# Performance work log

Hardware: AMD Instinct MI355X
Metric: run time of the kernel (lower is better)

Reference implementation:

```python
import jax, jax.numpy as jnp
import numpy as np

H = 16       # num_heads
DH = 64      # dim_head
SCALE = DH ** -0.5


def setup_inputs() -> dict:
    key = jax.random.key(0)
    k1, k2 = jax.random.split(key)
    ZT = jax.random.normal(k1, (2, 2048, 1024), dtype=jnp.float32)
    # Linear weight, shape (H*dh, dim); scaled like a typical init for stability
    W = jax.random.normal(k2, (1024, 1024), dtype=jnp.float32) * 0.02
    return {"ZT": ZT, "W": W}


def reference(ZT, W):
    b, n, dim = ZT.shape
    # UT(ZT): ZT @ W^T -> (b, n, H*dh), reshape to (b, h, n, dh)
    ZTU = jnp.einsum('bnd,ed->bne', ZT, W).reshape(b, n, H, DH).transpose(0, 2, 1, 3)
    # scores = ZTU @ ZTU^T * scale  (b, h, n, n)
    scores = jnp.einsum('bhnd,bhmd->bhnm', ZTU, ZTU) * SCALE
    attn = jax.nn.softmax(scores, axis=-1)  # dropout p=0 -> identity
    # attn @ ZTU -> (b, h, n, dh) -> (b, n, H*dh)
    ssa = jnp.einsum('bhnm,bhmd->bhnd', attn, ZTU)
    ssa = ssa.transpose(0, 2, 1, 3).reshape(b, n, H * DH)
    # UT(I).T == W (shape (H*dh, dim)); final projection back to dim
    mssa = jnp.einsum('bne,ed->bnd', ssa, W)
    # return_proj=False path: module returns (MSSA_out, MSSA_out)
    return (mssa, mssa)
```

## Files before the change

kernel.cpp:

```cpp
#include <hip/hip_runtime.h>
#include <hip/hip_bf16.h>
#include <stdint.h>

typedef __attribute__((ext_vector_type(8))) short bf16x8;
typedef __attribute__((ext_vector_type(4))) float f32x4;

#define MFMA16(a, b, c) __builtin_amdgcn_mfma_f32_16x16x32_bf16(a, b, c, 0, 0, 0)

typedef const __attribute__((address_space(1))) unsigned int* as1_u32p;
typedef __attribute__((address_space(3))) unsigned int* as3_u32p;
__device__ __forceinline__ void gl_lds16(const void* g, void* l) {
    __builtin_amdgcn_global_load_lds((as1_u32p)g, (as3_u32p)l, 16, 0, 0);
}

__device__ __forceinline__ unsigned short f2bs(float f) {
    __hip_bfloat16 h = __float2bfloat16(f);
    unsigned short s;
    __builtin_memcpy(&s, &h, 2);
    return s;
}

__device__ __forceinline__ unsigned int pk_bf16(float a, float b) {
    float2 f; f.x = a; f.y = b;
    __hip_bfloat162 h = __float22bfloat162_rn(f);
    unsigned int u;
    __builtin_memcpy(&u, &h, 4);
    return u;
}

__device__ __forceinline__ float exp2_raw(float x) {
    float r;
    asm("v_exp_f32 %0, %1" : "=v"(r) : "v"(x));
    return r;
}

#define QSCALE 0.18033688f

__global__ __launch_bounds__(256) void cvt_w_k(const float* __restrict__ w,
                                               unsigned short* __restrict__ wbf,
                                               unsigned short* __restrict__ wtbf) {
    __shared__ __attribute__((aligned(16))) unsigned short T[64 * 72];
    const int b2 = blockIdx.x;
    const int tid = threadIdx.x;
    const int e0 = (b2 >> 4) * 64, d0 = (b2 & 15) * 64;
    const int el = tid >> 2;
    const int dl = (tid & 3) * 16;
    const float* src = w + (size_t)(e0 + el) * 1024 + d0 + dl;
    unsigned short myv[16];
#pragma unroll
    for (int q = 0; q < 4; ++q) {
        const float4 v = *(const float4*)(src + q * 4);
        myv[q * 4 + 0] = f2bs(v.x);
        myv[q * 4 + 1] = f2bs(v.y);
        myv[q * 4 + 2] = f2bs(v.z);
        myv[q * 4 + 3] = f2bs(v.w);
    }
    *(bf16x8*)(wbf + (size_t)(e0 + el) * 1024 + d0 + dl) = *(const bf16x8*)&myv[0];
    *(bf16x8*)(wbf + (size_t)(e0 + el) * 1024 + d0 + dl + 8) = *(const bf16x8*)&myv[8];
#pragma unroll
    for (int q = 0; q < 16; ++q) T[(dl + q) * 72 + el] = myv[q];
    __syncthreads();
#pragma unroll
    for (int p = 0; p < 2; ++p) {
        const int idx = p * 256 + tid;
        const int dd = idx >> 3, c = (idx & 7) * 8;
        const bf16x8 v = *(const bf16x8*)&T[dd * 72 + c];
        *(bf16x8*)(wtbf + (size_t)(d0 + dd) * 1024 + e0 + c) = v;
    }
}

template <int EPI>
__global__ __launch_bounds__(256, 2) void gemm_bt_k(
    const float* __restrict__ Af32, const __hip_bfloat16* __restrict__ Abf,
    const __hip_bfloat16* __restrict__ B,
    unsigned short* __restrict__ ztu, unsigned short* __restrict__ ztut,
    float* __restrict__ out0, float* __restrict__ out1) {
    __shared__ __attribute__((aligned(16))) unsigned short smem[12288];
    unsigned short* At = smem;
    unsigned short* Bt = smem + 4096;
    unsigned short* Tb = smem;

    const int p = blockIdx.x;
    const int bm = (p & 7) * 8 + ((p >> 3) & 7);
    const int bn = p >> 6;
    const int tid = threadIdx.x;
    const int wave = tid >> 6, lane = tid & 63;
    const int wm = wave >> 1, wn = wave & 1;
    const int quad = lane >> 4, l16 = lane & 15;

    f32x4 acc[2][4] = {};

    const int lr = lane >> 2, lc = (lane & 3) * 8;
    const float* Agf = Af32 ? Af32 + (size_t)(bm * 64 + wave * 16 + lr) * 1024 + lc : nullptr;
    const __hip_bfloat16* Agb =
        Abf ? Abf + (size_t)(bm * 64 + wave * 16 + lr) * 1024 + lc : nullptr;
    const __hip_bfloat16* Bg0 = B + (size_t)(bn * 128 + (2 * wave) * 16 + lr) * 1024 + lc;
    const __hip_bfloat16* Bg1 = B + (size_t)(bn * 128 + (2 * wave + 1) * 16 + lr) * 1024 + lc;
    unsigned short* lA = At + wave * 512;
    unsigned short* lB0 = Bt + (2 * wave) * 512;
    unsigned short* lB1 = Bt + (2 * wave + 1) * 512;

    for (int kt = 0; kt < 16; ++kt) {
        const int ko = kt << 6;
        if (EPI == 0) {
#pragma unroll
            for (int h = 0; h < 2; ++h) {
                const float4 v0 = *(const float4*)(Agf + ko + h * 32);
                const float4 v1 = *(const float4*)(Agf + ko + h * 32 + 4);
                uint4 wv;
                wv.x = pk_bf16(v0.x, v0.y);
                wv.y = pk_bf16(v0.z, v0.w);
                wv.z = pk_bf16(v1.x, v1.y);
                wv.w = pk_bf16(v1.z, v1.w);
                *(uint4*)(lA + h * 2048 + lr * 32 + lc) = wv;
            }
        } else {
            gl_lds16(Agb + ko, lA);
            gl_lds16(Agb + ko + 32, lA + 2048);
        }
        gl_lds16(Bg0 + ko, lB0);
        gl_lds16(Bg0 + ko + 32, lB0 + 4096);
        gl_lds16(Bg1 + ko, lB1);
        gl_lds16(Bg1 + ko + 32, lB1 + 4096);
        __syncthreads();
        bf16x8 af[2][2], bfr[2][4];
#pragma unroll
        for (int h = 0; h < 2; ++h)
#pragma unroll
            for (int i = 0; i < 2; ++i)
                af[h][i] = *(const bf16x8*)&At[h * 2048 + (wm * 32 + i * 16 + l16) * 32 + quad * 8];
#pragma unroll
        for (int h = 0; h < 2; ++h)
#pragma unroll
            for (int j = 0; j < 4; ++j)
                bfr[h][j] = *(const bf16x8*)&Bt[h * 4096 + (wn * 64 + j * 16 + l16) * 32 + quad * 8];
#pragma unroll
        for (int h = 0; h < 2; ++h)
#pragma unroll
            for (int i = 0; i < 2; ++i)
#pragma unroll
                for (int j = 0; j < 4; ++j) acc[i][j] = MFMA16(af[h][i], bfr[h][j], acc[i][j]);
        __syncthreads();
    }

    if (EPI == 0) {
        const int h = bn * 2 + wn;
        const int bb = bm >> 5;
        const int nb = (bm & 31) * 64;
        const size_t hb = (size_t)(bb * 16 + h) * 131072;
#pragma unroll
        for (int i = 0; i < 2; ++i) {
#pragma unroll
            for (int r = 0; r < 4; ++r) {
                const int n = nb + wm * 32 + i * 16 + quad * 4 + r;
                uint2 pk;
                pk.x = pk_bf16(acc[i][0][r], acc[i][1][r]);
                pk.y = pk_bf16(acc[i][2][r], acc[i][3][r]);
                *(uint2*)(ztu + hb + n * 64 + l16 * 4) = pk;
                const int npl = wm * 32 + quad * 8 + i * 4 + r;
                Tb[(wn * 64 + 0 + l16) * 72 + npl] = (unsigned short)(pk.x & 0xffff);
                Tb[(wn * 64 + 16 + l16) * 72 + npl] = (unsigned short)(pk.x >> 16);
                Tb[(wn * 64 + 32 + l16) * 72 + npl] = (unsigned short)(pk.y & 0xffff);
                Tb[(wn * 64 + 48 + l16) * 72 + npl] = (unsigned short)(pk.y >> 16);
            }
        }
        __syncthreads();
#pragma unroll
        for (int ee = 0; ee < 4; ++ee) {
            const int e_local = wave * 32 + ee * 8 + (lane >> 3);
            const int nc = (lane & 7) * 8;
            const bf16x8 v = *(const bf16x8*)&Tb[e_local * 72 + nc];
            const int hh = bn * 2 + (e_local >> 6);
            const int dh = e_local & 63;
            *(bf16x8*)(ztut + (size_t)(bb * 16 + hh) * 131072 + dh * 2048 + nb + nc) = v;
        }
    } else {
#pragma unroll
        for (int i = 0; i < 2; ++i) {
#pragma unroll
            for (int r = 0; r < 4; ++r) {
                const int mm = bm * 64 + wm * 32 + i * 16 + quad * 4 + r;
#pragma unroll
                for (int j = 0; j < 4; ++j) {
                    const int e = bn * 128 + wn * 64 + j * 16 + l16;
                    const float v = acc[i][j][r];
                    out0[(size_t)mm * 1024 + e] = v;
                    out1[(size_t)mm * 1024 + e] = v;
                }
            }
        }
    }
}

__global__ __launch_bounds__(256, 2) void attn_k(const unsigned short* __restrict__ ztu,
                                                 const unsigned short* __restrict__ ztut,
                                                 unsigned short* __restrict__ ssa) {
    __shared__ __attribute__((aligned(16))) unsigned short Kt[64 * 64];
    __shared__ __attribute__((aligned(16))) unsigned short Vt[64 * 64];
    const int p = blockIdx.x;
    const int ii = p >> 3;
    const int bh = (p & 7) * 4 + (ii >> 4);
    const int qt = ii & 15;
    const int tid = threadIdx.x, wave = tid >> 6, lane = tid & 63;
    const int quad = lane >> 4, l16 = lane & 15;
    const unsigned short* base = ztu + (size_t)bh * 131072;
    const unsigned short* baseT = ztut + (size_t)bh * 131072;

    const int qb = qt * 128 + wave * 32;
    bf16x8 qa[2][2];
#pragma unroll
    for (int g = 0; g < 2; ++g) {
        qa[g][0] = *(const bf16x8*)(base + (qb + g * 16 + l16) * 64 + quad * 8);
        qa[g][1] = *(const bf16x8*)(base + (qb + g * 16 + l16) * 64 + 32 + quad * 8);
    }

    float lsum[2] = {0.f, 0.f};
    f32x4 o[2][4] = {};

    const int c0 = wave * 2, c1 = c0 + 1;
    const int lrow = lane >> 3;
    const int sw = (lane & 7) ^ lrow;
    const unsigned short* gK0 = base + (c0 * 8 + lrow) * 64 + sw * 8;
    const unsigned short* gK1 = base + (c1 * 8 + lrow) * 64 + sw * 8;
    const unsigned short* gV0 = baseT + (size_t)(c0 * 8 + lrow) * 2048 + sw * 8;
    const unsigned short* gV1 = baseT + (size_t)(c1 * 8 + lrow) * 2048 + sw * 8;
    unsigned short* lK0 = &Kt[c0 * 512];
    unsigned short* lK1 = &Kt[c1 * 512];
    unsigned short* lV0 = &Vt[c0 * 512];
    unsigned short* lV1 = &Vt[c1 * 512];

    const int swq = (quad ^ (l16 & 7));
    const int koff0 = l16 * 64 + swq * 8;
    const int koff1 = l16 * 64 + (swq ^ 4) * 8;

    for (int t = 0; t < 32; ++t) {
        gl_lds16(gK0 + t * 4096, lK0);
        gl_lds16(gK1 + t * 4096, lK1);
        gl_lds16(gV0 + t * 64, lV0);
        gl_lds16(gV1 + t * 64, lV1);
        __syncthreads();

        f32x4 st[2][4];
#pragma unroll
        for (int nf = 0; nf < 4; ++nf) {
            bf16x8 kb0 = *(const bf16x8*)&Kt[nf * 1024 + koff0];
            bf16x8 kb1 = *(const bf16x8*)&Kt[nf * 1024 + koff1];
#pragma unroll
            for (int g = 0; g < 2; ++g) {
                f32x4 z = {0.f, 0.f, 0.f, 0.f};
                z = MFMA16(kb0, qa[g][0], z);
                z = MFMA16(kb1, qa[g][1], z);
                st[g][nf] = z;
            }
        }

        bf16x8 pa[2][2];
#pragma unroll
        for (int g = 0; g < 2; ++g) {
            float e[16];
#pragma unroll
            for (int nf = 0; nf < 4; ++nf)
#pragma unroll
                for (int r = 0; r < 4; ++r) e[nf * 4 + r] = exp2_raw(st[g][nf][r] * QSCALE);
            float s0 = 0.f, s1 = 0.f;
#pragma unroll
            for (int q = 0; q < 8; ++q) { s0 += e[q]; s1 += e[q + 8]; }
            lsum[g] += s0 + s1;
            uint4 u0, u1;
            u0.x = pk_bf16(e[0], e[1]);   u0.y = pk_bf16(e[2], e[3]);
            u0.z = pk_bf16(e[4], e[5]);   u0.w = pk_bf16(e[6], e[7]);
            u1.x = pk_bf16(e[8], e[9]);   u1.y = pk_bf16(e[10], e[11]);
            u1.z = pk_bf16(e[12], e[13]); u1.w = pk_bf16(e[14], e[15]);
            __builtin_memcpy(&pa[g][0], &u0, 16);
            __builtin_memcpy(&pa[g][1], &u1, 16);
        }

#pragma unroll
        for (int df = 0; df < 4; ++df) {
            bf16x8 vb0 = *(const bf16x8*)&Vt[df * 1024 + koff0];
            bf16x8 vb1 = *(const bf16x8*)&Vt[df * 1024 + koff1];
#pragma unroll
            for (int g = 0; g < 2; ++g) {
                o[g][df] = MFMA16(vb0, pa[g][0], o[g][df]);
                o[g][df] = MFMA16(vb1, pa[g][1], o[g][df]);
            }
        }
        __syncthreads();
    }

    const int b = bh >> 4, h = bh & 15;
#pragma unroll
    for (int g = 0; g < 2; ++g) {
        float v = lsum[g];
        v += __shfl_xor(v, 16);
        v += __shfl_xor(v, 32);
        const float inv = 1.0f / v;
        const int token = b * 2048 + qb + g * 16 + l16;
#pragma unroll
        for (int df = 0; df < 4; ++df) {
            uint2 pk;
            pk.x = pk_bf16(o[g][df][0] * inv, o[g][df][1] * inv);
            pk.y = pk_bf16(o[g][df][2] * inv, o[g][df][3] * inv);
            *(uint2*)(ssa + (size_t)token * 1024 + h * 64 + df * 16 + quad * 4) = pk;
        }
    }
}

extern "C" void kernel_launch(void* const* d_in, const int* in_sizes, int n_in,
                              void* d_out, int out_size, void* d_ws, size_t ws_size,
                              hipStream_t stream) {
    const float* ZT = (const float*)d_in[0];
    const float* W = (const float*)d_in[1];
    float* out = (float*)d_out;
    char* ws = (char*)d_ws;

    unsigned short* wbf   = (unsigned short*)(ws);
    unsigned short* wtbf  = (unsigned short*)(ws + 2u * 1024 * 1024);
    unsigned short* ztu   = (unsigned short*)(ws + 4u * 1024 * 1024);
    unsigned short* ztut  = (unsigned short*)(ws + 12u * 1024 * 1024);
    unsigned short* ssabf = (unsigned short*)(ws + 20u * 1024 * 1024);

    cvt_w_k<<<256, 256, 0, stream>>>(W, wbf, wtbf);
    gemm_bt_k<0><<<512, 256, 0, stream>>>(ZT, nullptr, (const __hip_bfloat16*)wbf, ztu, ztut,
                                          nullptr, nullptr);
    attn_k<<<512, 256, 0, stream>>>(ztu, ztut, ssabf);
    gemm_bt_k<1><<<512, 256, 0, stream>>>(nullptr, (const __hip_bfloat16*)ssabf,
                                          (const __hip_bfloat16*)wtbf, nullptr, nullptr, out,
                                          out + 4194304);
}
```

Measured before the change: 158.7 us.

## Pre-convert ZT to bf16 and double-buffer swizzled LDS staging in GEMMs

ZT is now converted to bf16 in a widened conversion kernel, so the first GEMM can load A with direct global-to-LDS copies like the second GEMM. The GEMM main loop double-buffers LDS and prefetches the next K tile while computing the current one, using a 64-wide K tile with an XOR-swizzled layout to avoid bank conflicts. The cost is an extra fp32 read and bf16 write of ZT in a separate pass, plus twice the LDS per block, which may reduce occupancy.

```diff
diff --git a/kernel.cpp b/kernel.cpp
--- a/kernel.cpp
+++ b/kernel.cpp
@@ -36,12 +36,26 @@
 
 #define QSCALE 0.18033688f
 
-__global__ __launch_bounds__(256) void cvt_w_k(const float* __restrict__ w,
-                                               unsigned short* __restrict__ wbf,
-                                               unsigned short* __restrict__ wtbf) {
+__global__ __launch_bounds__(256) void cvt_k(const float* __restrict__ w,
+                                             const float* __restrict__ zt,
+                                             unsigned short* __restrict__ wbf,
+                                             unsigned short* __restrict__ wtbf,
+                                             unsigned short* __restrict__ ztbf) {
     __shared__ __attribute__((aligned(16))) unsigned short T[64 * 72];
+    const int tid = threadIdx.x;
+    if (blockIdx.x >= 256) {
+        const int i = ((int)blockIdx.x - 256) * 2048 + tid * 8;
+        const float4 v0 = *(const float4*)(zt + i);
+        const float4 v1 = *(const float4*)(zt + i + 4);
+        uint4 wv;
+        wv.x = pk_bf16(v0.x, v0.y);
+        wv.y = pk_bf16(v0.z, v0.w);
+        wv.z = pk_bf16(v1.x, v1.y);
+        wv.w = pk_bf16(v1.z, v1.w);
+        *(uint4*)(ztbf + i) = wv;
+        return;
+    }
     const int b2 = blockIdx.x;
-    const int tid = threadIdx.x;
     const int e0 = (b2 >> 4) * 64, d0 = (b2 & 15) * 64;
     const int el = tid >> 2;
     const int dl = (tid & 3) * 16;
@@ -71,13 +85,10 @@
 
 template <int EPI>
 __global__ __launch_bounds__(256, 2) void gemm_bt_k(
-    const float* __restrict__ Af32, const __hip_bfloat16* __restrict__ Abf,
-    const __hip_bfloat16* __restrict__ B,
+    const __hip_bfloat16* __restrict__ Abf, const __hip_bfloat16* __restrict__ B,
     unsigned short* __restrict__ ztu, unsigned short* __restrict__ ztut,
     float* __restrict__ out0, float* __restrict__ out1) {
-    __shared__ __attribute__((aligned(16))) unsigned short smem[12288];
-    unsigned short* At = smem;
-    unsigned short* Bt = smem + 4096;
+    __shared__ __attribute__((aligned(16))) unsigned short smem[24576];
     unsigned short* Tb = smem;
 
     const int p = blockIdx.x;
@@ -90,50 +101,46 @@
 
     f32x4 acc[2][4] = {};
 
-    const int lr = lane >> 2, lc = (lane & 3) * 8;
-    const float* Agf = Af32 ? Af32 + (size_t)(bm * 64 + wave * 16 + lr) * 1024 + lc : nullptr;
-    const __hip_bfloat16* Agb =
-        Abf ? Abf + (size_t)(bm * 64 + wave * 16 + lr) * 1024 + lc : nullptr;
-    const __hip_bfloat16* Bg0 = B + (size_t)(bn * 128 + (2 * wave) * 16 + lr) * 1024 + lc;
-    const __hip_bfloat16* Bg1 = B + (size_t)(bn * 128 + (2 * wave + 1) * 16 + lr) * 1024 + lc;
-    unsigned short* lA = At + wave * 512;
-    unsigned short* lB0 = Bt + (2 * wave) * 512;
-    unsigned short* lB1 = Bt + (2 * wave + 1) * 512;
+    const int lrow = lane >> 3;
+    const int sw = (lane & 7) ^ lrow;
+    const __hip_bfloat16* Ag0 = Abf + (size_t)(bm * 64 + (2 * wave) * 8 + lrow) * 1024 + sw * 8;
+    const __hip_bfloat16* Ag1 = Ag0 + 8 * 1024;
+    const __hip_bfloat16* Bg0 = B + (size_t)(bn * 128 + (4 * wave) * 8 + lrow) * 1024 + sw * 8;
+    const __hip_bfloat16* Bg1 = Bg0 + 8 * 1024;
+    const __hip_bfloat16* Bg2 = Bg0 + 16 * 1024;
+    const __hip_bfloat16* Bg3 = Bg0 + 24 * 1024;
+
+    auto stage = [&](int ko, unsigned short* sb) {
+        gl_lds16(Ag0 + ko, sb + (2 * wave) * 512);
+        gl_lds16(Ag1 + ko, sb + (2 * wave + 1) * 512);
+        gl_lds16(Bg0 + ko, sb + 4096 + (4 * wave) * 512);
+        gl_lds16(Bg1 + ko, sb + 4096 + (4 * wave + 1) * 512);
+        gl_lds16(Bg2 + ko, sb + 4096 + (4 * wave + 2) * 512);
+        gl_lds16(Bg3 + ko, sb + 4096 + (4 * wave + 3) * 512);
+    };
+
+    const int ch0 = (quad ^ (l16 & 7)) * 8;
+    const int ch1 = ch0 ^ 32;
+    const int raA = (wm * 32 + l16) * 64;
+    const int raB = (wn * 64 + l16) * 64;
+
+    stage(0, smem);
+    __syncthreads();
 
     for (int kt = 0; kt < 16; ++kt) {
-        const int ko = kt << 6;
-        if (EPI == 0) {
-#pragma unroll
-            for (int h = 0; h < 2; ++h) {
-                const float4 v0 = *(const float4*)(Agf + ko + h * 32);
-                const float4 v1 = *(const float4*)(Agf + ko + h * 32 + 4);
-                uint4 wv;
-                wv.x = pk_bf16(v0.x, v0.y);
-                wv.y = pk_bf16(v0.z, v0.w);
-                wv.z = pk_bf16(v1.x, v1.y);
-                wv.w = pk_bf16(v1.z, v1.w);
-                *(uint4*)(lA + h * 2048 + lr * 32 + lc) = wv;
-            }
-        } else {
-            gl_lds16(Agb + ko, lA);
-            gl_lds16(Agb + ko + 32, lA + 2048);
-        }
-        gl_lds16(Bg0 + ko, lB0);
-        gl_lds16(Bg0 + ko + 32, lB0 + 4096);
-        gl_lds16(Bg1 + ko, lB1);
-        gl_lds16(Bg1 + ko + 32, lB1 + 4096);
-        __syncthreads();
+        unsigned short* const sb = smem + (kt & 1) * 12288;
+        if (kt < 15) stage((kt + 1) << 6, smem + (((kt & 1) ^ 1) * 12288));
         bf16x8 af[2][2], bfr[2][4];
 #pragma unroll
-        for (int h = 0; h < 2; ++h)
-#pragma unroll
-            for (int i = 0; i < 2; ++i)
-                af[h][i] = *(const bf16x8*)&At[h * 2048 + (wm * 32 + i * 16 + l16) * 32 + quad * 8];
-#pragma unroll
-        for (int h = 0; h < 2; ++h)
-#pragma unroll
-            for (int j = 0; j < 4; ++j)
-                bfr[h][j] = *(const bf16x8*)&Bt[h * 4096 + (wn * 64 + j * 16 + l16) * 32 + quad * 8];
+        for (int i = 0; i < 2; ++i) {
+            af[0][i] = *(const bf16x8*)&sb[raA + i * 1024 + ch0];
+            af[1][i] = *(const bf16x8*)&sb[raA + i * 1024 + ch1];
+        }
+#pragma unroll
+        for (int j = 0; j < 4; ++j) {
+            bfr[0][j] = *(const bf16x8*)&sb[4096 + raB + j * 1024 + ch0];
+            bfr[1][j] = *(const bf16x8*)&sb[4096 + raB + j * 1024 + ch1];
+        }
 #pragma unroll
         for (int h = 0; h < 2; ++h)
 #pragma unroll
@@ -318,13 +325,14 @@
     unsigned short* wtbf  = (unsigned short*)(ws + 2u * 1024 * 1024);
     unsigned short* ztu   = (unsigned short*)(ws + 4u * 1024 * 1024);
     unsigned short* ztut  = (unsigned short*)(ws + 12u * 1024 * 1024);
-    unsigned short* ssabf = (unsigned short*)(ws + 20u * 1024 * 1024);
-
-    cvt_w_k<<<256, 256, 0, stream>>>(W, wbf, wtbf);
-    gemm_bt_k<0><<<512, 256, 0, stream>>>(ZT, nullptr, (const __hip_bfloat16*)wbf, ztu, ztut,
+    unsigned short* scr20 = (unsigned short*)(ws + 20u * 1024 * 1024);
+
+    cvt_k<<<2304, 256, 0, stream>>>(W, ZT, wbf, wtbf, scr20);
+    gemm_bt_k<0><<<512, 256, 0, stream>>>((const __hip_bfloat16*)scr20,
+                                          (const __hip_bfloat16*)wbf, ztu, ztut,
                                           nullptr, nullptr);
-    attn_k<<<512, 256, 0, stream>>>(ztu, ztut, ssabf);
-    gemm_bt_k<1><<<512, 256, 0, stream>>>(nullptr, (const __hip_bfloat16*)ssabf,
-                                          (const __hip_bfloat16*)wtbf, nullptr, nullptr, out,
-                                          out + 4194304);
-}
+    attn_k<<<512, 256, 0, stream>>>(ztu, ztut, scr20);
+    gemm_bt_k<1><<<512, 256, 0, stream>>>((const __hip_bfloat16*)scr20,
+                                          (const __hip_bfloat16*)wtbf, nullptr, nullptr,
+                                          out, out + 4194304);
+}
```

Measured after the change: 154.4 us. 1.03x faster.
